# Kernel tuning notes

Measured on AMD Instinct MI355X. Metric: run time of the kernel, lower is better.

Reference implementation:

```python
import jax, jax.numpy as jnp
import numpy as np

EPS = 1e-5
COMMITMENT_WEIGHT = 1.0


def setup_inputs() -> dict:
    key = jax.random.key(0)
    k1, k2 = jax.random.split(key)
    x = jax.random.normal(k1, (4, 4096, 128), dtype=jnp.float32)
    codebook = jax.random.normal(k2, (8192, 128), dtype=jnp.float32)
    return {"x": x, "codebook": codebook}


def _layernorm(x):
    # LayerNorm over last dim, elementwise_affine=False, eps=1e-5
    mu = jnp.mean(x, axis=-1, keepdims=True)
    var = jnp.mean(jnp.square(x - mu), axis=-1, keepdims=True)
    return (x - mu) * jax.lax.rsqrt(var + EPS)


def reference(x, codebook):
    b, n, d = x.shape
    xn = _layernorm(x)                      # [b, n, d]
    flat = xn.reshape(b * n, d)             # [bn, d]
    x2 = jnp.sum(flat * flat, axis=-1, keepdims=True)          # [bn, 1]
    e2 = jnp.sum(codebook * codebook, axis=-1)                  # [K]
    dots = jnp.einsum('nd,kd->nk', flat, codebook)              # [bn, K]
    distances = x2 - 2.0 * dots + e2[None, :]                   # [bn, K]
    embed_ind = jnp.argmin(distances, axis=-1)                  # [bn]
    quantize = codebook[embed_ind].reshape(b, n, d)             # gather
    embed_ind = embed_ind.reshape(b, n)
    loss = jnp.mean(jnp.square(quantize - xn)) * COMMITMENT_WEIGHT
    # straight-through
    quantize_st = xn + jax.lax.stop_gradient(quantize - xn)
    return (quantize_st, embed_ind, loss)
```

## Files before the change

### kernel.cpp

```cpp
#include <hip/hip_runtime.h>
#include <hip/hip_fp16.h>
#include <math.h>

typedef _Float16 half8  __attribute__((ext_vector_type(8)));
typedef _Float16 half2v __attribute__((ext_vector_type(2)));
typedef float   floatx4 __attribute__((ext_vector_type(4)));

#define ROWS   16384
#define DIM    128
#define KCODES 8192
#define NSPLIT 8
#define MTILE  512
#define NT     64
#define NCHUNK ((KCODES / NSPLIT) / NT)

__device__ __forceinline__ void async_copy16(const _Float16* src, _Float16* dst_lds) {
  __builtin_amdgcn_global_load_lds((const __attribute__((address_space(1))) void*)src,
                                   (__attribute__((address_space(3))) void*)dst_lds,
                                   16, 0, 0);
}

__global__ __launch_bounds__(256) void prep_codebook(
    const float* __restrict__ cb, _Float16* __restrict__ ehg,
    _Float16* __restrict__ elg, float* __restrict__ e2g)
{
  int tid = threadIdx.x;
  int L = tid & 63;
  int row = blockIdx.x * 4 + (tid >> 6);
  const float2* cr = (const float2*)(cb + (size_t)row * DIM);
  float2 v = cr[L];
  float s2 = v.x * v.x + v.y * v.y;
  #pragma unroll
  for (int m = 1; m < 64; m <<= 1) s2 += __shfl_xor(s2, m);
  if (L == 0) e2g[row] = s2;
  _Float16 h0 = (_Float16)v.x, h1 = (_Float16)v.y;
  half2v hi = {h0, h1};
  half2v lo = {(_Float16)(v.x - (float)h0), (_Float16)(v.y - (float)h1)};
  ((half2v*)(ehg + (size_t)row * DIM))[L] = hi;
  ((half2v*)(elg + (size_t)row * DIM))[L] = lo;
}

__global__ __launch_bounds__(512, 1) void argmin_kernel(
    const float* __restrict__ x, const _Float16* __restrict__ ehg,
    const _Float16* __restrict__ elg, const float* __restrict__ e2g,
    float* __restrict__ best_part, int* __restrict__ idx_part)
{
  __shared__ _Float16 ebuf[2][2][64][128];

  int tid = threadIdx.x;
  int w   = tid >> 6;
  int L   = tid & 63;
  int c   = L & 15;
  int q   = L >> 4;

  int bx = blockIdx.x;
  int mt = bx & (ROWS / MTILE - 1);
  int ns = bx >> 5;

  int rowbase = mt * MTILE + w * 64;

  half8 ah[4][4], al[4][4];

  #pragma unroll
  for (int g = 0; g < 4; ++g) {
    const float* xr = x + (size_t)(rowbase + g * 16 + c) * DIM;
    float v[32];
    #pragma unroll
    for (int ks = 0; ks < 4; ++ks) {
      float4 p0 = *(const float4*)(xr + ks * 32 + q * 8);
      float4 p1 = *(const float4*)(xr + ks * 32 + q * 8 + 4);
      v[ks*8+0] = p0.x; v[ks*8+1] = p0.y; v[ks*8+2] = p0.z; v[ks*8+3] = p0.w;
      v[ks*8+4] = p1.x; v[ks*8+5] = p1.y; v[ks*8+6] = p1.z; v[ks*8+7] = p1.w;
    }
    float s = 0.f;
    #pragma unroll
    for (int i = 0; i < 32; ++i) s += v[i];
    s += __shfl_xor(s, 16); s += __shfl_xor(s, 32);
    float mu = s * (1.0f / 128.0f);
    float s2 = 0.f;
    #pragma unroll
    for (int i = 0; i < 32; ++i) { float d = v[i] - mu; s2 += d * d; }
    s2 += __shfl_xor(s2, 16); s2 += __shfl_xor(s2, 32);
    float rstd = 1.0f / sqrtf(s2 * (1.0f / 128.0f) + 1e-5f);
    #pragma unroll
    for (int ks = 0; ks < 4; ++ks)
      #pragma unroll
      for (int j = 0; j < 8; ++j) {
        float xv = (v[ks*8+j] - mu) * rstd;
        _Float16 h = (_Float16)xv;
        ah[g][ks][j] = h;
        al[g][ks][j] = (_Float16)(xv - (float)h);
      }
  }

  float best[4][4]; int bidx[4][4];
  #pragma unroll
  for (int g = 0; g < 4; ++g)
    #pragma unroll
    for (int r = 0; r < 4; ++r) { best[g][r] = -3.4e38f; bidx[g][r] = 0; }

  int code0 = ns * (KCODES / NSPLIT);
  _Float16* lbase = &ebuf[0][0][0][0];

  auto stage = [&](int ch, int p) {
    int cbase = code0 + ch * NT;
    _Float16* lb = lbase + (size_t)p * 2 * 64 * 128;
    #pragma unroll
    for (int it = 0; it < 4; ++it) {
      int cid = it * 512 + tid;
      int arr = cid >> 10;
      int lc  = cid & 1023;
      int n   = lc >> 4;
      int kcs = lc & 15;
      int kc  = kcs ^ (n & 7);
      const _Float16* g = (arr ? elg : ehg) + (size_t)(cbase + n) * DIM + kc * 8;
      async_copy16(g, lb + (size_t)cid * 8);
    }
  };

  stage(0, 0);
  __syncthreads();

  for (int ch = 0; ch < NCHUNK; ++ch) {
    int p = ch & 1;
    int cbase = code0 + ch * NT;
    if (ch + 1 < NCHUNK) stage(ch + 1, p ^ 1);

    float e2h[4];
    #pragma unroll
    for (int s = 0; s < 4; ++s) e2h[s] = -0.5f * e2g[cbase + s * 16 + c];

    #pragma unroll
    for (int s = 0; s < 4; ++s) {
      int n = s * 16 + c;
      half8 bh[4], bl[4];
      #pragma unroll
      for (int ks = 0; ks < 4; ++ks) {
        int slot = ((ks * 4 + q) ^ (c & 7)) * 8;
        bh[ks] = *(const half8*)&ebuf[p][0][n][slot];
        bl[ks] = *(const half8*)&ebuf[p][1][n][slot];
      }
      int nn = cbase + n;
      #pragma unroll
      for (int g = 0; g < 4; ++g) {
        floatx4 acc = {e2h[s], e2h[s], e2h[s], e2h[s]};
        #pragma unroll
        for (int ks = 0; ks < 4; ++ks) {
          acc = __builtin_amdgcn_mfma_f32_16x16x32_f16(ah[g][ks], bh[ks], acc, 0, 0, 0);
          acc = __builtin_amdgcn_mfma_f32_16x16x32_f16(ah[g][ks], bl[ks], acc, 0, 0, 0);
          acc = __builtin_amdgcn_mfma_f32_16x16x32_f16(al[g][ks], bh[ks], acc, 0, 0, 0);
        }
        #pragma unroll
        for (int r = 0; r < 4; ++r) {
          float t = acc[r];
          if (t > best[g][r]) { best[g][r] = t; bidx[g][r] = nn; }
        }
      }
    }
    __syncthreads();
  }

  #pragma unroll
  for (int m = 1; m < 16; m <<= 1)
    #pragma unroll
    for (int g = 0; g < 4; ++g)
      #pragma unroll
      for (int r = 0; r < 4; ++r) {
        float ob = __shfl_xor(best[g][r], m);
        int   oi = __shfl_xor(bidx[g][r], m);
        if (ob > best[g][r] || (ob == best[g][r] && oi < bidx[g][r])) {
          best[g][r] = ob; bidx[g][r] = oi;
        }
      }
  if (c == 0) {
    #pragma unroll
    for (int g = 0; g < 4; ++g)
      #pragma unroll
      for (int r = 0; r < 4; ++r) {
        int row = rowbase + g * 16 + q * 4 + r;
        best_part[(size_t)row * NSPLIT + ns] = best[g][r];
        idx_part [(size_t)row * NSPLIT + ns] = bidx[g][r];
      }
  }
}

__global__ __launch_bounds__(256) void gather_loss_kernel(
    const float* __restrict__ x, const float* __restrict__ cb,
    const float* __restrict__ best_part, const int* __restrict__ idx_part,
    float* __restrict__ out_q, float* __restrict__ out_ind,
    float* __restrict__ row_loss)
{
  int tid = threadIdx.x;
  int L = tid & 63;
  int row = blockIdx.x * 4 + (tid >> 6);

  float b  = best_part[(size_t)row * NSPLIT + (L & 7)];
  int   bi = idx_part [(size_t)row * NSPLIT + (L & 7)];
  #pragma unroll
  for (int m = 1; m < 8; m <<= 1) {
    float ob = __shfl_xor(b, m);
    int   oi = __shfl_xor(bi, m);
    if (ob > b || (ob == b && oi < bi)) { b = ob; bi = oi; }
  }

  float2 qv = ((const float2*)(cb + (size_t)bi * DIM))[L];
  float2 xv = ((const float2*)(x  + (size_t)row * DIM))[L];
  float s = xv.x + xv.y;
  #pragma unroll
  for (int m = 1; m < 64; m <<= 1) s += __shfl_xor(s, m);
  float mu = s * (1.0f / 128.0f);
  float dx = xv.x - mu, dy = xv.y - mu;
  float s2 = dx * dx + dy * dy;
  #pragma unroll
  for (int m = 1; m < 64; m <<= 1) s2 += __shfl_xor(s2, m);
  float rstd = 1.0f / sqrtf(s2 * (1.0f / 128.0f) + 1e-5f);
  float xn0 = dx * rstd, xn1 = dy * rstd;
  ((float2*)out_q)[(size_t)row * 64 + L] = qv;
  float e0 = qv.x - xn0, e1 = qv.y - xn1;
  float le = e0 * e0 + e1 * e1;
  #pragma unroll
  for (int m = 1; m < 64; m <<= 1) le += __shfl_xor(le, m);
  if (L == 0) {
    row_loss[row] = le;
    out_ind[row] = (float)bi;
  }
}

__global__ __launch_bounds__(1024) void loss_reduce_kernel(
    const float* __restrict__ row_loss, float* __restrict__ out_loss)
{
  __shared__ float sm[1024];
  int tid = threadIdx.x;
  float s = 0.f;
  for (int i = tid; i < ROWS; i += 1024) s += row_loss[i];
  sm[tid] = s; __syncthreads();
  for (int st = 512; st > 0; st >>= 1) {
    if (tid < st) sm[tid] += sm[tid + st];
    __syncthreads();
  }
  if (tid == 0) *out_loss = sm[0] * (1.0f / (float)(ROWS * DIM));
}

extern "C" void kernel_launch(void* const* d_in, const int* in_sizes, int n_in,
                              void* d_out, int out_size, void* d_ws, size_t ws_size,
                              hipStream_t stream)
{
  const float* x  = (const float*)d_in[0];
  const float* cb = (const float*)d_in[1];

  char* ws = (char*)d_ws;
  _Float16* ehg      = (_Float16*)(ws + 0);
  _Float16* elg      = (_Float16*)(ws + 2097152);
  float*    e2g      = (float*)   (ws + 4194304);
  float*    best_part= (float*)   (ws + 4227072);
  int*      idx_part = (int*)     (ws + 4751360);
  float*    row_loss = (float*)   (ws + 5275648);

  float* out_q    = (float*)d_out;
  float* out_ind  = out_q + (size_t)ROWS * DIM;
  float* out_loss = out_ind + ROWS;

  prep_codebook<<<KCODES / 4, 256, 0, stream>>>(cb, ehg, elg, e2g);
  argmin_kernel<<<(ROWS / MTILE) * NSPLIT, 512, 0, stream>>>(x, ehg, elg, e2g, best_part, idx_part);
  gather_loss_kernel<<<ROWS / 4, 256, 0, stream>>>(x, cb, best_part, idx_part, out_q, out_ind, row_loss);
  loss_reduce_kernel<<<1, 1024, 0, stream>>>(row_loss, out_loss);
}
```

Baseline: 159.9 us.

## Double code split, raise occupancy, and derive loss algebraically from argmin scores

Doubles the codebook split to 16 with two blocks per CU allowed, caches the pre-scaled codebook norms in LDS, and has the argmin kernel emit per-row ||x||^2. The gather kernel then computes the commitment loss as x2 - 2*best instead of recomputing layernorm, and reduces it with an atomicAdd, eliminating the separate reduction kernel. The gather copy is also widened to float4. Risks include register spills under the tighter launch bound and a slight numerical change in the loss from using split-fp16 dot products.

```diff
diff --git a/kernel.cpp b/kernel.cpp
--- a/kernel.cpp
+++ b/kernel.cpp
@@ -9,10 +9,11 @@
 #define ROWS   16384
 #define DIM    128
 #define KCODES 8192
-#define NSPLIT 8
+#define NSPLIT 16
 #define MTILE  512
 #define NT     64
 #define NCHUNK ((KCODES / NSPLIT) / NT)
+#define LOSS_SCALE (1.0f / ((float)ROWS * (float)DIM))
 
 __device__ __forceinline__ void async_copy16(const _Float16* src, _Float16* dst_lds) {
   __builtin_amdgcn_global_load_lds((const __attribute__((address_space(1))) void*)src,
@@ -32,7 +33,7 @@
   float s2 = v.x * v.x + v.y * v.y;
   #pragma unroll
   for (int m = 1; m < 64; m <<= 1) s2 += __shfl_xor(s2, m);
-  if (L == 0) e2g[row] = s2;
+  if (L == 0) e2g[row] = -0.5f * s2;
   _Float16 h0 = (_Float16)v.x, h1 = (_Float16)v.y;
   half2v hi = {h0, h1};
   half2v lo = {(_Float16)(v.x - (float)h0), (_Float16)(v.y - (float)h1)};
@@ -40,12 +41,14 @@
   ((half2v*)(elg + (size_t)row * DIM))[L] = lo;
 }
 
-__global__ __launch_bounds__(512, 1) void argmin_kernel(
+__global__ __launch_bounds__(512, 2) void argmin_kernel(
     const float* __restrict__ x, const _Float16* __restrict__ ehg,
     const _Float16* __restrict__ elg, const float* __restrict__ e2g,
-    float* __restrict__ best_part, int* __restrict__ idx_part)
+    float* __restrict__ best_part, int* __restrict__ idx_part,
+    float* __restrict__ x2g)
 {
   __shared__ _Float16 ebuf[2][2][64][128];
+  __shared__ float e2s[KCODES / NSPLIT];
 
   int tid = threadIdx.x;
   int w   = tid >> 6;
@@ -54,10 +57,13 @@
   int q   = L >> 4;
 
   int bx = blockIdx.x;
-  int mt = bx & (ROWS / MTILE - 1);
+  int mt = bx & 31;
   int ns = bx >> 5;
 
   int rowbase = mt * MTILE + w * 64;
+  int code0 = ns * (KCODES / NSPLIT);
+
+  e2s[tid] = e2g[code0 + tid];
 
   half8 ah[4][4], al[4][4];
 
@@ -82,15 +88,19 @@
     for (int i = 0; i < 32; ++i) { float d = v[i] - mu; s2 += d * d; }
     s2 += __shfl_xor(s2, 16); s2 += __shfl_xor(s2, 32);
     float rstd = 1.0f / sqrtf(s2 * (1.0f / 128.0f) + 1e-5f);
+    float x2 = 0.f;
     #pragma unroll
     for (int ks = 0; ks < 4; ++ks)
       #pragma unroll
       for (int j = 0; j < 8; ++j) {
         float xv = (v[ks*8+j] - mu) * rstd;
+        x2 += xv * xv;
         _Float16 h = (_Float16)xv;
         ah[g][ks][j] = h;
         al[g][ks][j] = (_Float16)(xv - (float)h);
       }
+    x2 += __shfl_xor(x2, 16); x2 += __shfl_xor(x2, 32);
+    if (ns == 0 && q == 0) x2g[rowbase + g * 16 + c] = x2;
   }
 
   float best[4][4]; int bidx[4][4];
@@ -99,7 +109,6 @@
     #pragma unroll
     for (int r = 0; r < 4; ++r) { best[g][r] = -3.4e38f; bidx[g][r] = 0; }
 
-  int code0 = ns * (KCODES / NSPLIT);
   _Float16* lbase = &ebuf[0][0][0][0];
 
   auto stage = [&](int ch, int p) {
@@ -128,7 +137,7 @@
 
     float e2h[4];
     #pragma unroll
-    for (int s = 0; s < 4; ++s) e2h[s] = -0.5f * e2g[cbase + s * 16 + c];
+    for (int s = 0; s < 4; ++s) e2h[s] = e2s[ch * NT + s * 16 + c];
 
     #pragma unroll
     for (int s = 0; s < 4; ++s) {
@@ -185,60 +194,51 @@
 }
 
 __global__ __launch_bounds__(256) void gather_loss_kernel(
-    const float* __restrict__ x, const float* __restrict__ cb,
-    const float* __restrict__ best_part, const int* __restrict__ idx_part,
+    const float* __restrict__ cb, const float* __restrict__ best_part,
+    const int* __restrict__ idx_part, const float* __restrict__ x2g,
     float* __restrict__ out_q, float* __restrict__ out_ind,
-    float* __restrict__ row_loss)
-{
+    float* __restrict__ out_loss)
+{
+  __shared__ int   sidx[32];
+  __shared__ float sloss[32];
   int tid = threadIdx.x;
-  int L = tid & 63;
-  int row = blockIdx.x * 4 + (tid >> 6);
-
-  float b  = best_part[(size_t)row * NSPLIT + (L & 7)];
-  int   bi = idx_part [(size_t)row * NSPLIT + (L & 7)];
+  int rb = blockIdx.x * 32;
+  int r = tid >> 3, k = tid & 7;
+  int row = rb + r;
+
+  float b  = best_part[(size_t)row * NSPLIT + k];
+  int   bi = idx_part [(size_t)row * NSPLIT + k];
+  float b2 = best_part[(size_t)row * NSPLIT + 8 + k];
+  int   bj = idx_part [(size_t)row * NSPLIT + 8 + k];
+  if (b2 > b || (b2 == b && bj < bi)) { b = b2; bi = bj; }
   #pragma unroll
   for (int m = 1; m < 8; m <<= 1) {
     float ob = __shfl_xor(b, m);
     int   oi = __shfl_xor(bi, m);
     if (ob > b || (ob == b && oi < bi)) { b = ob; bi = oi; }
   }
-
-  float2 qv = ((const float2*)(cb + (size_t)bi * DIM))[L];
-  float2 xv = ((const float2*)(x  + (size_t)row * DIM))[L];
-  float s = xv.x + xv.y;
-  #pragma unroll
-  for (int m = 1; m < 64; m <<= 1) s += __shfl_xor(s, m);
-  float mu = s * (1.0f / 128.0f);
-  float dx = xv.x - mu, dy = xv.y - mu;
-  float s2 = dx * dx + dy * dy;
-  #pragma unroll
-  for (int m = 1; m < 64; m <<= 1) s2 += __shfl_xor(s2, m);
-  float rstd = 1.0f / sqrtf(s2 * (1.0f / 128.0f) + 1e-5f);
-  float xn0 = dx * rstd, xn1 = dy * rstd;
-  ((float2*)out_q)[(size_t)row * 64 + L] = qv;
-  float e0 = qv.x - xn0, e1 = qv.y - xn1;
-  float le = e0 * e0 + e1 * e1;
-  #pragma unroll
-  for (int m = 1; m < 64; m <<= 1) le += __shfl_xor(le, m);
-  if (L == 0) {
-    row_loss[row] = le;
+  if (k == 0) {
+    sidx[r] = bi;
     out_ind[row] = (float)bi;
-  }
-}
-
-__global__ __launch_bounds__(1024) void loss_reduce_kernel(
-    const float* __restrict__ row_loss, float* __restrict__ out_loss)
-{
-  __shared__ float sm[1024];
-  int tid = threadIdx.x;
-  float s = 0.f;
-  for (int i = tid; i < ROWS; i += 1024) s += row_loss[i];
-  sm[tid] = s; __syncthreads();
-  for (int st = 512; st > 0; st >>= 1) {
-    if (tid < st) sm[tid] += sm[tid + st];
-    __syncthreads();
-  }
-  if (tid == 0) *out_loss = sm[0] * (1.0f / (float)(ROWS * DIM));
+    sloss[r] = x2g[row] - 2.0f * b;
+  }
+  __syncthreads();
+
+  if (tid < 32) {
+    float s = sloss[tid];
+    #pragma unroll
+    for (int m = 1; m < 32; m <<= 1) s += __shfl_xor(s, m);
+    if (tid == 0) atomicAdd(out_loss, s * LOSS_SCALE);
+  }
+
+  const float4* cb4 = (const float4*)cb;
+  float4* oq4 = (float4*)out_q;
+  #pragma unroll
+  for (int it = 0; it < 4; ++it) {
+    int idx = it * 256 + tid;
+    int r2 = idx >> 5, c4 = idx & 31;
+    oq4[(size_t)(rb + r2) * 32 + c4] = cb4[(size_t)sidx[r2] * 32 + c4];
+  }
 }
 
 extern "C" void kernel_launch(void* const* d_in, const int* in_sizes, int n_in,
@@ -253,15 +253,15 @@
   _Float16* elg      = (_Float16*)(ws + 2097152);
   float*    e2g      = (float*)   (ws + 4194304);
   float*    best_part= (float*)   (ws + 4227072);
-  int*      idx_part = (int*)     (ws + 4751360);
-  float*    row_loss = (float*)   (ws + 5275648);
+  int*      idx_part = (int*)     (ws + 5275648);
+  float*    x2g      = (float*)   (ws + 6324224);
 
   float* out_q    = (float*)d_out;
   float* out_ind  = out_q + (size_t)ROWS * DIM;
   float* out_loss = out_ind + ROWS;
 
+  hipMemsetAsync(out_loss, 0, sizeof(float), stream);
   prep_codebook<<<KCODES / 4, 256, 0, stream>>>(cb, ehg, elg, e2g);
-  argmin_kernel<<<(ROWS / MTILE) * NSPLIT, 512, 0, stream>>>(x, ehg, elg, e2g, best_part, idx_part);
-  gather_loss_kernel<<<ROWS / 4, 256, 0, stream>>>(x, cb, best_part, idx_part, out_q, out_ind, row_loss);
-  loss_reduce_kernel<<<1, 1024, 0, stream>>>(row_loss, out_loss);
-}
+  argmin_kernel<<<(ROWS / MTILE) * NSPLIT, 512, 0, stream>>>(x, ehg, elg, e2g, best_part, idx_part, x2g);
+  gather_loss_kernel<<<ROWS / 32, 256, 0, stream>>>(cb, best_part, idx_part, x2g, out_q, out_ind, out_loss);
+}
```

Measured after the change: 172.2 us. 7.7% more time.
